# Kernel optimization log

Measured on AMD Instinct MI355X. Metric: run time of the kernel, lower is better.

## Reference

```python
import jax, jax.numpy as jnp
import numpy as np

NEG = -1e30  # log-space 'zero'


def _lse3(a, b, c):
    m = jnp.maximum(jnp.maximum(a, b), c)
    return m + jnp.log(jnp.exp(a - m) + jnp.exp(b - m) + jnp.exp(c - m))


def _ctc_loss_sum(logp, targets, input_lens, target_lens, blank=0):
    # logp: (T, B, C) log-probabilities; targets: (B, S) int; lens: (B,) int
    T, B, C = logp.shape
    S = targets.shape[1]
    L = 2 * S + 1
    # Extended label sequence: blank, t0, blank, t1, ..., blank  -> (B, L)
    ext = jnp.full((B, L), blank, dtype=targets.dtype).at[:, 1::2].set(targets)
    # Skip transition (l-2 -> l) allowed only for non-blank labels differing from l-2
    allow_skip = jnp.concatenate(
        [jnp.zeros((B, 2), bool), (ext[:, 2:] != blank) & (ext[:, 2:] != ext[:, :-2])],
        axis=1)  # (B, L)
    pos = jnp.arange(L)[None, :]
    valid = pos < (2 * target_lens[:, None] + 1)  # (B, L) mask of used trellis columns

    def emit(lp_t):  # (B, C) -> (B, L): log-prob of emitting ext label at each position
        return jnp.take_along_axis(lp_t, ext, axis=1)

    e0 = emit(logp[0])
    alpha0 = jnp.full((B, L), NEG, logp.dtype).at[:, 0].set(e0[:, 0]).at[:, 1].set(e0[:, 1])
    alpha0 = jnp.where(valid, alpha0, NEG)

    def step(alpha, lp_t):
        a1 = jnp.pad(alpha[:, :-1], ((0, 0), (1, 0)), constant_values=NEG)
        a2 = jnp.pad(alpha[:, :-2], ((0, 0), (2, 0)), constant_values=NEG)
        a2 = jnp.where(allow_skip, a2, NEG)
        new = _lse3(alpha, a1, a2) + emit(lp_t)
        new = jnp.where(valid, new, NEG)
        return new, new

    _, alphas = jax.lax.scan(step, alpha0, logp[1:])
    alphas = jnp.concatenate([alpha0[None], alphas], axis=0)  # (T, B, L)

    # Per-sequence final alpha at t = input_len - 1
    a_fin = alphas[input_lens - 1, jnp.arange(B)]  # (B, L)
    end_blank = jnp.take_along_axis(a_fin, (2 * target_lens)[:, None], axis=1)[:, 0]
    end_label = jnp.take_along_axis(a_fin, (2 * target_lens - 1)[:, None], axis=1)[:, 0]
    m = jnp.maximum(end_blank, end_label)
    loss = -(m + jnp.log(jnp.exp(end_blank - m) + jnp.exp(end_label - m)))  # (B,)
    # zero_infinity=True: replace (near-)infinite losses with 0
    loss = jnp.where(loss > -0.5 * NEG, 0.0, loss)
    # reduction='none' followed by .sum() in the module
    return loss.sum()


def setup_inputs() -> dict:
    key = jax.random.key(0)
    T, B, C, S = 1000, 32, 1000, 100
    k1, k2 = jax.random.split(key)
    logits = jax.random.normal(k1, (T, B, C), dtype=jnp.float32)
    logp = jax.nn.log_softmax(logits, axis=-1)  # CTCLoss expects log-softmax input
    targets = jax.random.randint(k2, (B, S), 1, C)  # labels in [1, C), never blank(0)
    input_lens = jnp.full((B,), T, dtype=jnp.int32)
    target_lens = jnp.full((B,), S, dtype=jnp.int32)
    return {"logp": logp, "targets": targets, "input_lens": input_lens, "target_lens": target_lens}


def reference(logp, targets, input_lens, target_lens):
    return _ctc_loss_sum(logp, targets, input_lens, target_lens, blank=0)
```

## Files before the change

### kernel.cpp

```cpp
#include <hip/hip_runtime.h>


constexpr int T = 1000, B = 32, C = 1000, S = 100;
constexpr int L = 2 * S + 1;
constexpr int RS = 204;
constexpr int PFD = 32;
constexpr int RROWS = T + PFD;
constexpr float OFF = 7.0f;
constexpr float LOG2E = 1.4426950408889634f;
constexpr float LN2 = 0.6931471805599453f;

__device__ __forceinline__ float dpp_shr1(float x) {
    return __int_as_float(
        __builtin_amdgcn_update_dpp(0, __float_as_int(x), 0x138, 0xF, 0xF, true));
}

__device__ __forceinline__ float wave_max_nonneg(float x) {
#define DPP_MAX(ctrl)                                                        \
    x = fmaxf(x, __int_as_float(__builtin_amdgcn_update_dpp(                 \
                     0, __float_as_int(x), (ctrl), 0xF, 0xF, true)))
    DPP_MAX(0x111);
    DPP_MAX(0x112);
    DPP_MAX(0x114);
    DPP_MAX(0x118);
    DPP_MAX(0x142);
    DPP_MAX(0x143);
#undef DPP_MAX
    return __int_as_float(__builtin_amdgcn_readlane(__float_as_int(x), 63));
}

__global__ void stage_kernel(const float* __restrict__ logp,
                             const int* __restrict__ targets,
                             float* __restrict__ ws) {
    const int t = blockIdx.x;
    const int b = blockIdx.y;
    __shared__ float row[C];
    const float* src = logp + ((size_t)t * B + b) * C;
    const int tid = threadIdx.x;
    if (tid < C / 4) {
        ((float4*)row)[tid] = ((const float4*)src)[tid];
    }
    __syncthreads();
    if (tid < RS) {
        float p;
        if (tid < L) {
            const int c = (tid & 1) ? targets[b * S + (tid >> 1)] : 0;
            p = exp2f((row[c] + OFF) * LOG2E);
        } else {
            p = 0.0f;
        }
        ws[((size_t)b * RROWS + t) * RS + tid] = p;
    }
}

__global__ void __launch_bounds__(64) ctc_kernel(const float* __restrict__ ws,
                                                 const int* __restrict__ targets,
                                                 const int* __restrict__ input_lens,
                                                 const int* __restrict__ target_lens,
                                                 float* __restrict__ out) {
    const int b = blockIdx.x;
    const int lane = threadIdx.x;
    const int col = (lane <= 50) ? 4 * lane : 200;
    const int Tb = input_lens[b];
    const int tl = target_lens[b];
    const float* pw = ws + (size_t)b * RROWS * RS;

    float m1 = 0.f, m3 = 0.f;
    if (lane <= 50) {
        const int l1 = col + 1;
        if (l1 >= 3 && l1 < L) {
            const int s = (l1 - 1) >> 1;
            if (targets[b * S + s] != targets[b * S + s - 1]) m1 = 1.f;
        }
        const int l3 = col + 3;
        if (l3 >= 3 && l3 < L) {
            const int s = (l3 - 1) >> 1;
            if (targets[b * S + s] != targets[b * S + s - 1]) m3 = 1.f;
        }
    }

    float a0 = 0.f, a1 = 0.f, a2 = 0.f, a3 = 0.f;
    {
        const float4 p0 = *(const float4*)(pw + col);
        if (lane == 0) { a0 = p0.x; a1 = p0.y; }
    }
    int esum = 0;

#define CTC_STEP(P_)                                  \
    do {                                              \
        const float am1 = dpp_shr1(a3);               \
        const float s01 = a0 + a1;                    \
        const float s23 = a2 + a3;                    \
        const float n0 = (a0 + am1) * (P_).x;         \
        const float n1 = fmaf(am1, m1, s01) * (P_).y; \
        const float n2 = (a1 + a2) * (P_).z;          \
        const float n3 = fmaf(a1, m3, s23) * (P_).w;  \
        a0 = n0; a1 = n1; a2 = n2; a3 = n3;           \
    } while (0)

#define CTC_RESCALE()                                                          \
    do {                                                                       \
        const float mx = wave_max_nonneg(fmaxf(fmaxf(a0, a1), fmaxf(a2, a3))); \
        const unsigned bits = __float_as_uint(mx);                             \
        if (bits != 0u) {                                                      \
            const int e = (int)((bits >> 23) & 0xFFu) - 127;                   \
            const float sc = __uint_as_float((unsigned)(127 - e) << 23);       \
            a0 *= sc; a1 *= sc; a2 *= sc; a3 *= sc;                            \
            esum += e;                                                         \
        }                                                                      \
    } while (0)

    float4 P[PFD];
    {
        const float* pf0 = pw + (size_t)RS + col;
#pragma unroll
        for (int i = 0; i < PFD; ++i) P[i] = *(const float4*)(pf0 + (size_t)i * RS);
    }
    const float* pf = pw + (size_t)(PFD + 1) * RS + col;

    int t = 1;
    while (t + PFD <= Tb) {
#pragma unroll
        for (int i = 0; i < PFD; ++i) {
            const float4 p = P[i];
            P[i] = *(const float4*)pf;
            pf += RS;
            CTC_STEP(p);
            if (i == 15) CTC_RESCALE();
        }
        CTC_RESCALE();
        t += PFD;
    }
    {
        const int rem = Tb - t;
#pragma unroll
        for (int i = 0; i < PFD; ++i) {
            if (i < rem) {
                const float4 p = P[i];
                CTC_STEP(p);
            }
        }
    }
#undef CTC_STEP

    const int e1 = 2 * tl, e2 = 2 * tl - 1;
    float contrib = 0.f;
    if (lane <= 50) {
        if (col + 0 == e1 || col + 0 == e2) contrib += a0;
        if (col + 1 == e1 || col + 1 == e2) contrib += a1;
        if (col + 2 == e1 || col + 2 == e2) contrib += a2;
        if (col + 3 == e1 || col + 3 == e2) contrib += a3;
    }
#pragma unroll
    for (int off = 32; off; off >>= 1) contrib += __shfl_xor(contrib, off);

    if (lane == 0) {
        const float logalpha = logf(contrib) + (float)esum * LN2 - OFF * (float)Tb;
        float loss = -logalpha;
        if (!(loss < 0.5e30f)) loss = 0.f;
        atomicAdd(out, loss);
    }
}

__global__ void __launch_bounds__(64) ctc_direct_kernel(const float* __restrict__ logp,
                                                        const int* __restrict__ targets,
                                                        const int* __restrict__ input_lens,
                                                        const int* __restrict__ target_lens,
                                                        float* __restrict__ out) {
    const int b = blockIdx.x;
    const int lane = threadIdx.x;
    const int col = (lane <= 50) ? 4 * lane : 200;
    const int Tb = input_lens[b];
    const int tl = target_lens[b];

    int cc[4]; float mm[4], pm[4];
#pragma unroll
    for (int i = 0; i < 4; ++i) {
        const int l = col + i;
        const bool real = (lane <= 50) && (l < L);
        pm[i] = real ? 1.f : 0.f;
        cc[i] = real ? ((l & 1) ? targets[b * S + (l >> 1)] : 0) : 0;
        float mk = 0.f;
        if (real && (l & 1) && l >= 3) {
            const int s = (l - 1) >> 1;
            if (targets[b * S + s] != targets[b * S + s - 1]) mk = 1.f;
        }
        mm[i] = mk;
    }
    const float m1 = mm[1], m3 = mm[3];

    float a0 = 0.f, a1 = 0.f, a2 = 0.f, a3 = 0.f;
    {
        const float* rowp = logp + (size_t)b * C;
        const float p0 = pm[0] * exp2f((rowp[cc[0]] + OFF) * LOG2E);
        const float p1 = pm[1] * exp2f((rowp[cc[1]] + OFF) * LOG2E);
        if (lane == 0) { a0 = p0; a1 = p1; }
    }
    int esum = 0;

    for (int t = 1; t < Tb; ++t) {
        const float* rowp = logp + ((size_t)t * B + b) * C;
        const float p0 = pm[0] * exp2f((rowp[cc[0]] + OFF) * LOG2E);
        const float p1 = pm[1] * exp2f((rowp[cc[1]] + OFF) * LOG2E);
        const float p2 = pm[2] * exp2f((rowp[cc[2]] + OFF) * LOG2E);
        const float p3 = pm[3] * exp2f((rowp[cc[3]] + OFF) * LOG2E);
        const float am1 = dpp_shr1(a3);
        const float n0 = (a0 + am1) * p0;
        const float n1 = fmaf(am1, m1, a0 + a1) * p1;
        const float n2 = (a1 + a2) * p2;
        const float n3 = fmaf(a1, m3, a2 + a3) * p3;
        a0 = n0; a1 = n1; a2 = n2; a3 = n3;
        if ((t & 15) == 0) {
            const float mx = wave_max_nonneg(fmaxf(fmaxf(a0, a1), fmaxf(a2, a3)));
            const unsigned bits = __float_as_uint(mx);
            if (bits != 0u) {
                const int e = (int)((bits >> 23) & 0xFFu) - 127;
                const float sc = __uint_as_float((unsigned)(127 - e) << 23);
                a0 *= sc; a1 *= sc; a2 *= sc; a3 *= sc;
                esum += e;
            }
        }
    }

    const int e1 = 2 * tl, e2 = 2 * tl - 1;
    float contrib = 0.f;
    if (lane <= 50) {
        if (col + 0 == e1 || col + 0 == e2) contrib += a0;
        if (col + 1 == e1 || col + 1 == e2) contrib += a1;
        if (col + 2 == e1 || col + 2 == e2) contrib += a2;
        if (col + 3 == e1 || col + 3 == e2) contrib += a3;
    }
#pragma unroll
    for (int off = 32; off; off >>= 1) contrib += __shfl_xor(contrib, off);
    if (lane == 0) {
        const float logalpha = logf(contrib) + (float)esum * LN2 - OFF * (float)Tb;
        float loss = -logalpha;
        if (!(loss < 0.5e30f)) loss = 0.f;
        atomicAdd(out, loss);
    }
}

extern "C" void kernel_launch(void* const* d_in, const int* in_sizes, int n_in,
                              void* d_out, int out_size, void* d_ws, size_t ws_size,
                              hipStream_t stream) {
    const float* logp = (const float*)d_in[0];
    const int* targets = (const int*)d_in[1];
    const int* input_lens = (const int*)d_in[2];
    const int* target_lens = (const int*)d_in[3];
    float* out = (float*)d_out;
    float* ws = (float*)d_ws;

    hipMemsetAsync(d_out, 0, sizeof(float), stream);

    const size_t ws_needed = (size_t)B * RROWS * RS * sizeof(float);
    if (ws_size >= ws_needed) {
        dim3 gA(T, B);
        stage_kernel<<<gA, 256, 0, stream>>>(logp, targets, ws);
        ctc_kernel<<<B, 64, 0, stream>>>(ws, targets, input_lens, target_lens, out);
    } else {
        ctc_direct_kernel<<<B, 64, 0, stream>>>(logp, targets, input_lens, target_lens, out);
    }
}
```

Before: 236.1 us.

## Fuse staging and CTC recursion into one producer-consumer kernel with LDS ring

Replaces the two-kernel design (a global staging kernel that writes exp'd emission rows to workspace, then a one-wave recursion kernel) with a single kernel per batch element. Fourteen producer waves stream logp rows from global memory using inline-asm double-buffered loads, convert each row to fp16 in LDS, gather the label columns, and write exp'd probabilities into a 40-slot LDS ring guarded by flags. Wave 0 spins on those flags and runs the alpha recursion eight steps at a time. This removes the workspace round trip and the second launch, at the cost of spin-wait synchronisation, fp16 rounding of the log-probs, and only 32 blocks on the device.

```diff
diff --git a/kernel.cpp b/kernel.cpp
--- a/kernel.cpp
+++ b/kernel.cpp
@@ -1,11 +1,12 @@
 #include <hip/hip_runtime.h>
-
-
-constexpr int T = 1000, B = 32, C = 1000, S = 100;
-constexpr int L = 2 * S + 1;
-constexpr int RS = 204;
-constexpr int PFD = 32;
-constexpr int RROWS = T + PFD;
+#include <hip/hip_fp16.h>
+
+
+constexpr int Bc = 32, Cc = 1000, Sc = 100;
+constexpr int L = 2 * Sc + 1;
+constexpr int NP = 14;
+constexpr int RING = 40;
+constexpr int RSF = 204;
 constexpr float OFF = 7.0f;
 constexpr float LOG2E = 1.4426950408889634f;
 constexpr float LN2 = 0.6931471805599453f;
@@ -19,72 +20,73 @@
 #define DPP_MAX(ctrl)                                                        \
     x = fmaxf(x, __int_as_float(__builtin_amdgcn_update_dpp(                 \
                      0, __float_as_int(x), (ctrl), 0xF, 0xF, true)))
-    DPP_MAX(0x111);
-    DPP_MAX(0x112);
-    DPP_MAX(0x114);
-    DPP_MAX(0x118);
-    DPP_MAX(0x142);
-    DPP_MAX(0x143);
+    DPP_MAX(0x111); DPP_MAX(0x112); DPP_MAX(0x114);
+    DPP_MAX(0x118); DPP_MAX(0x142); DPP_MAX(0x143);
 #undef DPP_MAX
     return __int_as_float(__builtin_amdgcn_readlane(__float_as_int(x), 63));
 }
 
-__global__ void stage_kernel(const float* __restrict__ logp,
-                             const int* __restrict__ targets,
-                             float* __restrict__ ws) {
-    const int t = blockIdx.x;
-    const int b = blockIdx.y;
-    __shared__ float row[C];
-    const float* src = logp + ((size_t)t * B + b) * C;
+__device__ __forceinline__ void issue_row(uint4& r0, uint4& r1, uint4& r2,
+                                          uint4& r3, const float* p) {
+    asm volatile(
+        "global_load_dwordx4 %0, %4, off\n\t"
+        "global_load_dwordx4 %1, %4, off offset:16\n\t"
+        "global_load_dwordx4 %2, %4, off offset:32\n\t"
+        "global_load_dwordx4 %3, %4, off offset:48"
+        : "=v"(r0), "=v"(r1), "=v"(r2), "=v"(r3)
+        : "v"(p));
+}
+__device__ __forceinline__ void wait4(uint4& r0, uint4& r1, uint4& r2, uint4& r3) {
+    asm volatile("s_waitcnt vmcnt(4)"
+                 : "+v"(r0.x), "+v"(r0.y), "+v"(r0.z), "+v"(r0.w),
+                   "+v"(r1.x), "+v"(r1.y), "+v"(r1.z), "+v"(r1.w),
+                   "+v"(r2.x), "+v"(r2.y), "+v"(r2.z), "+v"(r2.w),
+                   "+v"(r3.x), "+v"(r3.y), "+v"(r3.z), "+v"(r3.w));
+}
+
+__global__ void __launch_bounds__(960, 4) ctc_fused(
+        const float* __restrict__ logp, const int* __restrict__ targets,
+        const int* __restrict__ input_lens, const int* __restrict__ target_lens,
+        float* __restrict__ out) {
+    __shared__ __half scratch[NP][1024];
+    __shared__ float ring[RING * RSF];
+    __shared__ int flags[RING];
+    __shared__ int consp;
+
+    const int b = blockIdx.x;
     const int tid = threadIdx.x;
-    if (tid < C / 4) {
-        ((float4*)row)[tid] = ((const float4*)src)[tid];
-    }
-    __syncthreads();
-    if (tid < RS) {
-        float p;
-        if (tid < L) {
-            const int c = (tid & 1) ? targets[b * S + (tid >> 1)] : 0;
-            p = exp2f((row[c] + OFF) * LOG2E);
-        } else {
-            p = 0.0f;
-        }
-        ws[((size_t)b * RROWS + t) * RS + tid] = p;
-    }
-}
-
-__global__ void __launch_bounds__(64) ctc_kernel(const float* __restrict__ ws,
-                                                 const int* __restrict__ targets,
-                                                 const int* __restrict__ input_lens,
-                                                 const int* __restrict__ target_lens,
-                                                 float* __restrict__ out) {
-    const int b = blockIdx.x;
-    const int lane = threadIdx.x;
-    const int col = (lane <= 50) ? 4 * lane : 200;
+    const int wid = tid >> 6;
+    const int lane = tid & 63;
     const int Tb = input_lens[b];
     const int tl = target_lens[b];
-    const float* pw = ws + (size_t)b * RROWS * RS;
-
-    float m1 = 0.f, m3 = 0.f;
-    if (lane <= 50) {
-        const int l1 = col + 1;
-        if (l1 >= 3 && l1 < L) {
-            const int s = (l1 - 1) >> 1;
-            if (targets[b * S + s] != targets[b * S + s - 1]) m1 = 1.f;
-        }
-        const int l3 = col + 3;
-        if (l3 >= 3 && l3 < L) {
-            const int s = (l3 - 1) >> 1;
-            if (targets[b * S + s] != targets[b * S + s - 1]) m3 = 1.f;
-        }
-    }
-
-    float a0 = 0.f, a1 = 0.f, a2 = 0.f, a3 = 0.f;
-    {
-        const float4 p0 = *(const float4*)(pw + col);
-        if (lane == 0) { a0 = p0.x; a1 = p0.y; }
-    }
-    int esum = 0;
+
+    if (tid < RING) flags[tid] = -1;
+    if (tid == RING) consp = -1;
+    __syncthreads();
+
+    volatile int* vflags = flags;
+    volatile int* vconsp = &consp;
+
+    if (wid == 0) {
+        const int col = (lane <= 50) ? 4 * lane : 200;
+        const int lcl = (lane <= 50) ? lane : 50;
+
+        float m1 = 0.f, m3 = 0.f;
+        if (lane <= 50) {
+            const int l1 = col + 1;
+            if (l1 >= 3 && l1 < L) {
+                const int s = (l1 - 1) >> 1;
+                if (targets[b * Sc + s] != targets[b * Sc + s - 1]) m1 = 1.f;
+            }
+            const int l3 = col + 3;
+            if (l3 >= 3 && l3 < L) {
+                const int s = (l3 - 1) >> 1;
+                if (targets[b * Sc + s] != targets[b * Sc + s - 1]) m3 = 1.f;
+            }
+        }
+
+        float a0 = 0.f, a1 = 0.f, a2 = 0.f, a3 = 0.f;
+        int esum = 0;
 
 #define CTC_STEP(P_)                                  \
     do {                                              \
@@ -110,133 +112,146 @@
         }                                                                      \
     } while (0)
 
-    float4 P[PFD];
-    {
-        const float* pf0 = pw + (size_t)RS + col;
-#pragma unroll
-        for (int i = 0; i < PFD; ++i) P[i] = *(const float4*)(pf0 + (size_t)i * RS);
-    }
-    const float* pf = pw + (size_t)(PFD + 1) * RS + col;
-
-    int t = 1;
-    while (t + PFD <= Tb) {
-#pragma unroll
-        for (int i = 0; i < PFD; ++i) {
-            const float4 p = P[i];
-            P[i] = *(const float4*)pf;
-            pf += RS;
-            CTC_STEP(p);
-            if (i == 15) CTC_RESCALE();
-        }
-        CTC_RESCALE();
-        t += PFD;
-    }
-    {
-        const int rem = Tb - t;
-#pragma unroll
-        for (int i = 0; i < PFD; ++i) {
-            if (i < rem) {
-                const float4 p = P[i];
-                CTC_STEP(p);
+        while (vflags[0] != 0) {}
+        __threadfence_block();
+        {
+            const float4 q0 = *(const float4*)&ring[4 * lcl];
+            if (lane == 0) { a0 = q0.x; a1 = q0.y; }
+        }
+
+        int t = 1, since = 0;
+        while (t + 8 <= Tb) {
+            const int k = lane & 7;
+            const int idx = (t + k) % RING;
+            const int want = t + k;
+            while (!__all(vflags[idx] == want)) {}
+            __threadfence_block();
+            float4 q[8];
+#pragma unroll
+            for (int j = 0; j < 8; ++j)
+                q[j] = *(const float4*)&ring[((t + j) % RING) * RSF + 4 * lcl];
+#pragma unroll
+            for (int j = 0; j < 8; ++j) CTC_STEP(q[j]);
+            since += 8;
+            if (since >= 16) { CTC_RESCALE(); since = 0; }
+            if (lane == 0) *vconsp = t + 7;
+            t += 8;
+        }
+        for (; t < Tb; ++t) {
+            const int idx = t % RING;
+            while (vflags[idx] != t) {}
+            __threadfence_block();
+            const float4 q = *(const float4*)&ring[idx * RSF + 4 * lcl];
+            CTC_STEP(q);
+        }
+#undef CTC_STEP
+
+        const int e1 = 2 * tl, e2 = 2 * tl - 1;
+        float contrib = 0.f;
+        if (lane <= 50) {
+            if (col + 0 == e1 || col + 0 == e2) contrib += a0;
+            if (col + 1 == e1 || col + 1 == e2) contrib += a1;
+            if (col + 2 == e1 || col + 2 == e2) contrib += a2;
+            if (col + 3 == e1 || col + 3 == e2) contrib += a3;
+        }
+#pragma unroll
+        for (int off = 32; off; off >>= 1) contrib += __shfl_xor(contrib, off);
+
+        if (lane == 0) {
+            const float logalpha =
+                logf(contrib) + (float)esum * LN2 - OFF * (float)Tb;
+            float loss = -logalpha;
+            if (!(loss < 0.5e30f)) loss = 0.f;
+            atomicAdd(out, loss);
+        }
+    } else {
+        const int p = wid - 1;
+
+        int cof[4];
+#pragma unroll
+        for (int j = 0; j < 4; ++j) {
+            const int g = lane + 64 * j;
+            int c = 0;
+            if (g < L && (g & 1)) c = targets[b * Sc + (g >> 1)];
+            cof[j] = c;
+        }
+        const int basecol = (16 * lane < Cc - 16) ? 16 * lane : (Cc - 16);
+        asm volatile("s_waitcnt vmcnt(0)" ::: "memory");
+
+        uint4 A0, A1, A2, A3, B0, B1, B2, B3;
+
+#define PROC_ROW(R0_, R1_, R2_, R3_, T_)                                      \
+    do {                                                                      \
+        uint4 x, y;                                                           \
+        {                                                                     \
+            __half2 h0, h1, h2, h3, h4, h5, h6, h7;                           \
+            const float* fa = (const float*)&(R0_);                           \
+            const float* fb = (const float*)&(R1_);                           \
+            const float* fc = (const float*)&(R2_);                           \
+            const float* fd = (const float*)&(R3_);                           \
+            h0.x = __float2half(fa[0]); h0.y = __float2half(fa[1]);           \
+            h1.x = __float2half(fa[2]); h1.y = __float2half(fa[3]);           \
+            h2.x = __float2half(fb[0]); h2.y = __float2half(fb[1]);           \
+            h3.x = __float2half(fb[2]); h3.y = __float2half(fb[3]);           \
+            h4.x = __float2half(fc[0]); h4.y = __float2half(fc[1]);           \
+            h5.x = __float2half(fc[2]); h5.y = __float2half(fc[3]);           \
+            h6.x = __float2half(fd[0]); h6.y = __float2half(fd[1]);           \
+            h7.x = __float2half(fd[2]); h7.y = __float2half(fd[3]);           \
+            x.x = *(unsigned*)&h0; x.y = *(unsigned*)&h1;                     \
+            x.z = *(unsigned*)&h2; x.w = *(unsigned*)&h3;                     \
+            y.x = *(unsigned*)&h4; y.y = *(unsigned*)&h5;                     \
+            y.z = *(unsigned*)&h6; y.w = *(unsigned*)&h7;                     \
+        }                                                                     \
+        if (lane < 63) {                                                      \
+            uint4* dst = (uint4*)&scratch[p][basecol];                        \
+            dst[0] = x; dst[1] = y;                                           \
+        }                                                                     \
+        const int slot_ = (T_) % RING;                                        \
+        float* rr = &ring[slot_ * RSF];                                       \
+        _Pragma("unroll")                                                     \
+        for (int j = 0; j < 4; ++j) {                                         \
+            const int g = lane + 64 * j;                                      \
+            if (g < RSF) {                                                    \
+                float pv = 0.f;                                               \
+                if (g < L) {                                                  \
+                    const float lp = __half2float(scratch[p][cof[j]]);        \
+                    pv = exp2f((lp + OFF) * LOG2E);                           \
+                }                                                             \
+                rr[g] = pv;                                                   \
+            }                                                                 \
+        }                                                                     \
+        __threadfence_block();                                                \
+        if (lane == 0) vflags[slot_] = (T_);                                  \
+    } while (0)
+
+        int t = p;
+        if (t < Tb) {
+            issue_row(A0, A1, A2, A3,
+                      logp + ((size_t)t * Bc + b) * Cc + basecol);
+            while (true) {
+                while ((t - *vconsp) > RING) {}
+                {
+                    const int tn = (t + NP < Tb) ? t + NP : t;
+                    issue_row(B0, B1, B2, B3,
+                              logp + ((size_t)tn * Bc + b) * Cc + basecol);
+                }
+                wait4(A0, A1, A2, A3);
+                PROC_ROW(A0, A1, A2, A3, t);
+                t += NP;
+                if (t >= Tb) break;
+                while ((t - *vconsp) > RING) {}
+                {
+                    const int tn = (t + NP < Tb) ? t + NP : t;
+                    issue_row(A0, A1, A2, A3,
+                              logp + ((size_t)tn * Bc + b) * Cc + basecol);
+                }
+                wait4(B0, B1, B2, B3);
+                PROC_ROW(B0, B1, B2, B3, t);
+                t += NP;
+                if (t >= Tb) break;
             }
         }
-    }
-#undef CTC_STEP
-
-    const int e1 = 2 * tl, e2 = 2 * tl - 1;
-    float contrib = 0.f;
-    if (lane <= 50) {
-        if (col + 0 == e1 || col + 0 == e2) contrib += a0;
-        if (col + 1 == e1 || col + 1 == e2) contrib += a1;
-        if (col + 2 == e1 || col + 2 == e2) contrib += a2;
-        if (col + 3 == e1 || col + 3 == e2) contrib += a3;
-    }
-#pragma unroll
-    for (int off = 32; off; off >>= 1) contrib += __shfl_xor(contrib, off);
-
-    if (lane == 0) {
-        const float logalpha = logf(contrib) + (float)esum * LN2 - OFF * (float)Tb;
-        float loss = -logalpha;
-        if (!(loss < 0.5e30f)) loss = 0.f;
-        atomicAdd(out, loss);
-    }
-}
-
-__global__ void __launch_bounds__(64) ctc_direct_kernel(const float* __restrict__ logp,
-                                                        const int* __restrict__ targets,
-                                                        const int* __restrict__ input_lens,
-                                                        const int* __restrict__ target_lens,
-                                                        float* __restrict__ out) {
-    const int b = blockIdx.x;
-    const int lane = threadIdx.x;
-    const int col = (lane <= 50) ? 4 * lane : 200;
-    const int Tb = input_lens[b];
-    const int tl = target_lens[b];
-
-    int cc[4]; float mm[4], pm[4];
-#pragma unroll
-    for (int i = 0; i < 4; ++i) {
-        const int l = col + i;
-        const bool real = (lane <= 50) && (l < L);
-        pm[i] = real ? 1.f : 0.f;
-        cc[i] = real ? ((l & 1) ? targets[b * S + (l >> 1)] : 0) : 0;
-        float mk = 0.f;
-        if (real && (l & 1) && l >= 3) {
-            const int s = (l - 1) >> 1;
-            if (targets[b * S + s] != targets[b * S + s - 1]) mk = 1.f;
-        }
-        mm[i] = mk;
-    }
-    const float m1 = mm[1], m3 = mm[3];
-
-    float a0 = 0.f, a1 = 0.f, a2 = 0.f, a3 = 0.f;
-    {
-        const float* rowp = logp + (size_t)b * C;
-        const float p0 = pm[0] * exp2f((rowp[cc[0]] + OFF) * LOG2E);
-        const float p1 = pm[1] * exp2f((rowp[cc[1]] + OFF) * LOG2E);
-        if (lane == 0) { a0 = p0; a1 = p1; }
-    }
-    int esum = 0;
-
-    for (int t = 1; t < Tb; ++t) {
-        const float* rowp = logp + ((size_t)t * B + b) * C;
-        const float p0 = pm[0] * exp2f((rowp[cc[0]] + OFF) * LOG2E);
-        const float p1 = pm[1] * exp2f((rowp[cc[1]] + OFF) * LOG2E);
-        const float p2 = pm[2] * exp2f((rowp[cc[2]] + OFF) * LOG2E);
-        const float p3 = pm[3] * exp2f((rowp[cc[3]] + OFF) * LOG2E);
-        const float am1 = dpp_shr1(a3);
-        const float n0 = (a0 + am1) * p0;
-        const float n1 = fmaf(am1, m1, a0 + a1) * p1;
-        const float n2 = (a1 + a2) * p2;
-        const float n3 = fmaf(a1, m3, a2 + a3) * p3;
-        a0 = n0; a1 = n1; a2 = n2; a3 = n3;
-        if ((t & 15) == 0) {
-            const float mx = wave_max_nonneg(fmaxf(fmaxf(a0, a1), fmaxf(a2, a3)));
-            const unsigned bits = __float_as_uint(mx);
-            if (bits != 0u) {
-                const int e = (int)((bits >> 23) & 0xFFu) - 127;
-                const float sc = __uint_as_float((unsigned)(127 - e) << 23);
-                a0 *= sc; a1 *= sc; a2 *= sc; a3 *= sc;
-                esum += e;
-            }
-        }
-    }
-
-    const int e1 = 2 * tl, e2 = 2 * tl - 1;
-    float contrib = 0.f;
-    if (lane <= 50) {
-        if (col + 0 == e1 || col + 0 == e2) contrib += a0;
-        if (col + 1 == e1 || col + 1 == e2) contrib += a1;
-        if (col + 2 == e1 || col + 2 == e2) contrib += a2;
-        if (col + 3 == e1 || col + 3 == e2) contrib += a3;
-    }
-#pragma unroll
-    for (int off = 32; off; off >>= 1) contrib += __shfl_xor(contrib, off);
-    if (lane == 0) {
-        const float logalpha = logf(contrib) + (float)esum * LN2 - OFF * (float)Tb;
-        float loss = -logalpha;
-        if (!(loss < 0.5e30f)) loss = 0.f;
-        atomicAdd(out, loss);
+#undef PROC_ROW
     }
 }
 
@@ -248,16 +263,8 @@
     const int* input_lens = (const int*)d_in[2];
     const int* target_lens = (const int*)d_in[3];
     float* out = (float*)d_out;
-    float* ws = (float*)d_ws;
-
-    hipMemsetAsync(d_out, 0, sizeof(float), stream);
-
-    const size_t ws_needed = (size_t)B * RROWS * RS * sizeof(float);
-    if (ws_size >= ws_needed) {
-        dim3 gA(T, B);
-        stage_kernel<<<gA, 256, 0, stream>>>(logp, targets, ws);
-        ctc_kernel<<<B, 64, 0, stream>>>(ws, targets, input_lens, target_lens, out);
-    } else {
-        ctc_direct_kernel<<<B, 64, 0, stream>>>(logp, targets, input_lens, target_lens, out);
-    }
-}
+    (void)d_ws; (void)ws_size; (void)in_sizes; (void)n_in; (void)out_size;
+
+    (void)hipMemsetAsync(d_out, 0, sizeof(float), stream);
+    ctc_fused<<<Bc, 960, 0, stream>>>(logp, targets, input_lens, target_lens, out);
+}
```

After: 261.2 us. 1.11x slower.
